# Performance work log

Hardware: AMD Instinct MI355X
Metric: run time of the kernel (lower is better)

## Reference

```python
import jax, jax.numpy as jnp
import numpy as np
import math

D_MODEL = 1024
NUM_HEADS = 16


def setup_inputs() -> dict:
    key = jax.random.key(0)
    k1, k2, k3 = jax.random.split(key, 3)
    x = jax.random.normal(k1, (4, 2048, D_MODEL), dtype=jnp.float32)
    scale = 1.0 / math.sqrt(D_MODEL)
    W_qkv = jax.random.normal(k2, (3 * D_MODEL, D_MODEL), dtype=jnp.float32) * scale
    W_out = jax.random.normal(k3, (D_MODEL, D_MODEL), dtype=jnp.float32) * scale
    return {"x": x, "W_qkv": W_qkv, "W_out": W_out}


def reference(x, W_qkv, W_out):
    B, S, D = x.shape
    H = NUM_HEADS
    hd = D // H
    qkv = x @ W_qkv.T                      # [B,S,3D]
    q, k, v = jnp.split(qkv, 3, axis=-1)
    # [B,S,D] -> [B,H,S,hd]
    q = q.reshape(B, S, H, hd).transpose(0, 2, 1, 3)
    k = k.reshape(B, S, H, hd).transpose(0, 2, 1, 3)
    v = v.reshape(B, S, H, hd).transpose(0, 2, 1, 3)
    scores = jnp.einsum('bhqd,bhkd->bhqk', q, k) / math.sqrt(hd)
    causal = jnp.tril(jnp.ones((S, S), dtype=bool))
    scores = jnp.where(causal, scores, -jnp.inf)
    w = jax.nn.softmax(scores, axis=-1)
    out = jnp.einsum('bhqk,bhkd->bhqd', w, v)
    out = out.transpose(0, 2, 1, 3).reshape(B, S, D)
    return out @ W_out.T
```

## Files before the change

### kernel.cpp

```cpp
#include <hip/hip_runtime.h>
#include <hip/hip_bf16.h>
#include <stdint.h>


typedef __bf16 bf16_t;
typedef __attribute__((ext_vector_type(8))) __bf16 bf16x8;
typedef __attribute__((ext_vector_type(4))) __bf16 bf16x4;
typedef __attribute__((ext_vector_type(4))) float f32x4;

#define LOG2E 1.44269504088896340736f
#define SCLF (0.125f * LOG2E)
#define MFMA16(a, b, c) __builtin_amdgcn_mfma_f32_16x16x32_bf16(a, b, c, 0, 0, 0)

__device__ __forceinline__ bf16x8 ld8(const bf16_t* p) {
    return *(const bf16x8*)p;
}
__device__ __forceinline__ bf16x8 cvt8(const float* p) {
    f32x4 a = *(const f32x4*)p;
    f32x4 b = *(const f32x4*)(p + 4);
    bf16x8 r;
    r[0] = (bf16_t)a[0]; r[1] = (bf16_t)a[1]; r[2] = (bf16_t)a[2]; r[3] = (bf16_t)a[3];
    r[4] = (bf16_t)b[0]; r[5] = (bf16_t)b[1]; r[6] = (bf16_t)b[2]; r[7] = (bf16_t)b[3];
    return r;
}

__device__ __forceinline__ bool probe_f32(const void* w) {
    const uint16_t* u = (const uint16_t*)w;
    int cnt = 0;
#pragma unroll
    for (int i = 0; i < 64; ++i) {
        const int e = (u[i] >> 7) & 0xFF;
        cnt += (e >= 96 && e <= 150) ? 1 : 0;
    }
    return cnt < 56;
}

__device__ __forceinline__ void gll16(const bf16_t* g, bf16_t* l) {
    __builtin_amdgcn_global_load_lds(
        (const __attribute__((address_space(1))) void*)g,
        (__attribute__((address_space(3))) void*)l, 16, 0, 0);
}

__global__ __launch_bounds__(256) void cvt_big_kernel(
    const void* __restrict__ x, const void* __restrict__ wq,
    bf16_t* __restrict__ xb, bf16_t* __restrict__ wqb)
{
    const int gid = blockIdx.x * 256 + threadIdx.x;
    const void* src;
    bf16_t* dst;
    int off;
    if (gid < 1048576) { src = x;  dst = xb;  off = gid; }
    else               { src = wq; dst = wqb; off = gid - 1048576; }
    const bool f32 = probe_f32(src);
    const bf16x8 v = f32 ? cvt8((const float*)src + (size_t)off * 8)
                         : ld8((const bf16_t*)src + (size_t)off * 8);
    *(bf16x8*)(dst + (size_t)off * 8) = v;
}

__global__ __launch_bounds__(256) void cvt_small_kernel(
    const void* __restrict__ wo, bf16_t* __restrict__ wob)
{
    const int off = blockIdx.x * 256 + threadIdx.x;
    const bool f32 = probe_f32(wo);
    const bf16x8 v = f32 ? cvt8((const float*)wo + (size_t)off * 8)
                         : ld8((const bf16_t*)wo + (size_t)off * 8);
    *(bf16x8*)(wob + (size_t)off * 8) = v;
}

template <int EPI>
__global__ __launch_bounds__(256) void gemm_bt_lds(
    const bf16_t* __restrict__ A, const bf16_t* __restrict__ B,
    void* __restrict__ C, bf16_t* __restrict__ VT,
    int M, int N, int K)
{
    __shared__ __align__(16) bf16_t lsA[128 * 32];
    __shared__ __align__(16) bf16_t lsB[128 * 32];

    const int t    = threadIdx.x;
    const int lane = t & 63;
    const int wid  = t >> 6;
    const int quad = lane >> 4;
    const int l15  = lane & 15;
    const int wm   = (wid & 1) * 64;
    const int wn   = (wid >> 1) * 64;
    const int m0   = blockIdx.y * 128;
    const int n0   = blockIdx.x * 128;

    const bf16_t* Ar = A + (size_t)(m0 + (t >> 2)) * K + (t & 3) * 8;
    const bf16_t* Br = B + (size_t)(n0 + (t >> 2)) * K + (t & 3) * 8;
    bf16_t* la = lsA + t * 8;
    bf16_t* lb = lsB + t * 8;

    f32x4 acc[4][4];
#pragma unroll
    for (int i = 0; i < 4; ++i)
#pragma unroll
        for (int j = 0; j < 4; ++j) acc[i][j] = (f32x4){0.f, 0.f, 0.f, 0.f};

    for (int k0 = 0; k0 < K; k0 += 32) {
        __syncthreads();
        gll16(Ar + k0, la);
        gll16(Ar + (size_t)64 * K + k0, la + 2048);
        gll16(Br + k0, lb);
        gll16(Br + (size_t)64 * K + k0, lb + 2048);
        __syncthreads();

        bf16x8 af[4], bfr[4];
#pragma unroll
        for (int i = 0; i < 4; ++i)
            af[i] = ld8(lsA + (wm + i * 16 + l15) * 32 + quad * 8);
#pragma unroll
        for (int j = 0; j < 4; ++j)
            bfr[j] = ld8(lsB + (wn + j * 16 + l15) * 32 + quad * 8);
#pragma unroll
        for (int i = 0; i < 4; ++i)
#pragma unroll
            for (int j = 0; j < 4; ++j)
                acc[i][j] = MFMA16(af[i], bfr[j], acc[i][j]);
    }

#pragma unroll
    for (int i = 0; i < 4; ++i) {
        const int row = m0 + wm + i * 16 + quad * 4;
#pragma unroll
        for (int j = 0; j < 4; ++j) {
            const int col = n0 + wn + j * 16 + l15;
#pragma unroll
            for (int r = 0; r < 4; ++r) {
                const int rr = row + r;
                if (EPI == 0) {
                    ((float*)C)[(size_t)rr * N + col] = acc[i][j][r];
                } else {
                    const bf16_t v = (bf16_t)acc[i][j][r];
                    if (col < 2048) {
                        ((bf16_t*)C)[(size_t)rr * 2048 + col] = v;
                    } else {
                        const int c2 = col - 2048;
                        const int h = c2 >> 6, d = c2 & 63;
                        const int b = rr >> 11, s = rr & 2047;
                        VT[((size_t)((b << 4) + h) * 64 + d) * 2048 + s] = v;
                    }
                }
            }
        }
    }
}

struct Kfrag { bf16x8 k00, k01, k10, k11; };

__device__ __forceinline__ Kfrag ldk(const bf16_t* Kbase, int key0) {
    const bf16_t* kp = Kbase + (size_t)key0 * 2048;
    Kfrag f;
    f.k00 = ld8(kp);
    f.k01 = ld8(kp + 32);
    f.k10 = ld8(kp + (size_t)16 * 2048);
    f.k11 = ld8(kp + (size_t)16 * 2048 + 32);
    return f;
}

__device__ __forceinline__ bf16x4 expq(f32x4 s, float& lsum) {
    bf16x4 r;
#pragma unroll
    for (int i = 0; i < 4; ++i) {
        const float e = exp2f(s[i] * SCLF);
        r[i] = (bf16_t)e;
        lsum += (float)r[i];
    }
    return r;
}
__device__ __forceinline__ bf16x4 expq_m(f32x4 s, float& lsum, int quad, int l15) {
    bf16x4 r;
#pragma unroll
    for (int i = 0; i < 4; ++i) {
        const float e = (quad * 4 + i <= l15) ? exp2f(s[i] * SCLF) : 0.f;
        r[i] = (bf16_t)e;
        lsum += (float)r[i];
    }
    return r;
}

typedef union { bf16x4 h; int u[2]; } pk2;
typedef union { int u[4]; bf16x8 v; } pk4u;

__device__ __forceinline__ bf16x8 xpose(bf16x4 p0, bf16x4 p1, int s0b, int s1b, bool lowsel) {
    pk2 a, b;
    a.h = p0; b.h = p1;
    const int x0 = __builtin_amdgcn_ds_bpermute(s0b, a.u[0]);
    const int y0 = __builtin_amdgcn_ds_bpermute(s0b, b.u[0]);
    const int x1 = __builtin_amdgcn_ds_bpermute(s0b, a.u[1]);
    const int y1 = __builtin_amdgcn_ds_bpermute(s0b, b.u[1]);
    const int x2 = __builtin_amdgcn_ds_bpermute(s1b, a.u[0]);
    const int y2 = __builtin_amdgcn_ds_bpermute(s1b, b.u[0]);
    const int x3 = __builtin_amdgcn_ds_bpermute(s1b, a.u[1]);
    const int y3 = __builtin_amdgcn_ds_bpermute(s1b, b.u[1]);
    pk4u r;
    r.u[0] = lowsel ? x0 : y0;
    r.u[1] = lowsel ? x1 : y1;
    r.u[2] = lowsel ? x2 : y2;
    r.u[3] = lowsel ? x3 : y3;
    return r.v;
}

template <int DIAG>
__device__ __forceinline__ void attn_step(
    const Kfrag& kf, const bf16_t* __restrict__ Vbase, int key0,
    int quad, int l15, int s0b, int s1b, bool lowsel,
    const bf16x8& qa0, const bf16x8& qa1, const bf16x8& qb0, const bf16x8& qb1,
    f32x4 (&oa)[4], f32x4 (&ob)[4], float& la, float& lb)
{
    const bf16_t* vp = Vbase + key0;
    const bf16x8 vf0 = ld8(vp);
    const bf16x8 vf1 = ld8(vp + (size_t)16 * 2048);
    const bf16x8 vf2 = ld8(vp + (size_t)32 * 2048);
    const bf16x8 vf3 = ld8(vp + (size_t)48 * 2048);

    const f32x4 Z = (f32x4){0.f, 0.f, 0.f, 0.f};
    f32x4 s0a = Z, s1a = Z, s0b_ = Z, s1b_ = Z;
    s0a = MFMA16(kf.k00, qa0, s0a); s0a = MFMA16(kf.k01, qa1, s0a);
    s0b_ = MFMA16(kf.k00, qb0, s0b_); s0b_ = MFMA16(kf.k01, qb1, s0b_);
    if (!DIAG) {
        s1a = MFMA16(kf.k10, qa0, s1a); s1a = MFMA16(kf.k11, qa1, s1a);
    }
    s1b_ = MFMA16(kf.k10, qb0, s1b_); s1b_ = MFMA16(kf.k11, qb1, s1b_);

    bf16x4 pa0, pa1, pb0, pb1;
    if (DIAG) {
        pa0 = expq_m(s0a, la, quad, l15);
        pa1 = (bf16x4){(bf16_t)0.f, (bf16_t)0.f, (bf16_t)0.f, (bf16_t)0.f};
        pb0 = expq(s0b_, lb);
        pb1 = expq_m(s1b_, lb, quad, l15);
    } else {
        pa0 = expq(s0a, la); pa1 = expq(s1a, la);
        pb0 = expq(s0b_, lb); pb1 = expq(s1b_, lb);
    }

    const bf16x8 pfa = xpose(pa0, pa1, s0b, s1b, lowsel);
    const bf16x8 pfb = xpose(pb0, pb1, s0b, s1b, lowsel);

    oa[0] = MFMA16(pfa, vf0, oa[0]); ob[0] = MFMA16(pfb, vf0, ob[0]);
    oa[1] = MFMA16(pfa, vf1, oa[1]); ob[1] = MFMA16(pfb, vf1, ob[1]);
    oa[2] = MFMA16(pfa, vf2, oa[2]); ob[2] = MFMA16(pfb, vf2, ob[2]);
    oa[3] = MFMA16(pfa, vf3, oa[3]); ob[3] = MFMA16(pfb, vf3, ob[3]);
}

__global__ __launch_bounds__(128) void attn_kernel(
    const bf16_t* __restrict__ qk, const bf16_t* __restrict__ vt,
    bf16_t* __restrict__ out)
{
    __shared__ float mrg[64][34];

    const int t    = threadIdx.x;
    const int par  = t >> 6;
    const int lane = t & 63;
    const int quad = lane >> 4;
    const int l15  = lane & 15;

    const int bx = blockIdx.x;
    const int u  = bx & 255;
    const int v_ = bx >> 8;

    const int bh = ((u & 15) << 2) | (v_ & 3);
    const int c  = u >> 4;
    const int q2 = v_ >> 2;
    const int cc = (q2 & 1) ? (15 - c) : c;
    const int qt = (q2 << 4) | cc;
    const int b  = bh >> 4;
    const int h  = bh & 15;
    const int q0 = qt << 5;

    const int s0b = ((((quad << 1)) & 3) * 16 + l15) << 2;
    const int s1b = ((((quad << 1) + 1) & 3) * 16 + l15) << 2;
    const bool lowsel = quad < 2;

    const bf16_t* Qp = qk + (size_t)(b * 2048 + q0 + l15) * 2048 + h * 64 + quad * 8;
    const bf16x8 qa0 = ld8(Qp);
    const bf16x8 qa1 = ld8(Qp + 32);
    const bf16x8 qb0 = ld8(Qp + (size_t)16 * 2048);
    const bf16x8 qb1 = ld8(Qp + (size_t)16 * 2048 + 32);

    const bf16_t* Kbase = qk + (size_t)(b * 2048 + l15) * 2048 + 1024 + h * 64 + quad * 8;
    const bf16_t* Vbase = vt + ((size_t)bh * 64 + l15) * 2048 + quad * 8;

    f32x4 oa[4], ob[4];
#pragma unroll
    for (int v = 0; v < 4; ++v) {
        oa[v] = (f32x4){0.f, 0.f, 0.f, 0.f};
        ob[v] = (f32x4){0.f, 0.f, 0.f, 0.f};
    }
    float la = 0.f, lb = 0.f;

    const bool dg = ((qt & 1) == par);
    int kb = par;
    if (kb < qt || dg) {
        Kfrag kc = ldk(Kbase, ((kb < qt) ? kb : qt) << 5);
        while (kb < qt) {
            const int nk = (kb + 2 < qt) ? (kb + 2) : qt;
            Kfrag kn = ldk(Kbase, nk << 5);
            attn_step<0>(kc, Vbase, kb << 5, quad, l15, s0b, s1b, lowsel,
                         qa0, qa1, qb0, qb1, oa, ob, la, lb);
            kc = kn;
            kb += 2;
        }
        if (dg)
            attn_step<1>(kc, Vbase, qt << 5, quad, l15, s0b, s1b, lowsel,
                         qa0, qa1, qb0, qb1, oa, ob, la, lb);
    }

    float* m = &mrg[lane][0];
    if (par == 1) {
#pragma unroll
        for (int v = 0; v < 4; ++v)
#pragma unroll
            for (int r = 0; r < 4; ++r) {
                m[v * 4 + r]      = oa[v][r];
                m[16 + v * 4 + r] = ob[v][r];
            }
        m[32] = la; m[33] = lb;
    }
    __syncthreads();
    if (par == 1) return;

#pragma unroll
    for (int v = 0; v < 4; ++v)
#pragma unroll
        for (int r = 0; r < 4; ++r) {
            oa[v][r] += m[v * 4 + r];
            ob[v][r] += m[16 + v * 4 + r];
        }
    la += m[32]; lb += m[33];

    la += __shfl_xor(la, 16); la += __shfl_xor(la, 32);
    lb += __shfl_xor(lb, 16); lb += __shfl_xor(lb, 32);
    const float inva = 1.0f / la;
    const float invb = 1.0f / lb;

    const size_t obase = (size_t)(b * 2048 + q0 + quad * 4) * 1024 + h * 64 + l15;
#pragma unroll
    for (int r = 0; r < 4; ++r) {
        const float ia = __shfl(inva, quad * 4 + r);
        const float ib = __shfl(invb, quad * 4 + r);
#pragma unroll
        for (int v = 0; v < 4; ++v) {
            out[obase + (size_t)r * 1024 + v * 16]        = (bf16_t)(oa[v][r] * ia);
            out[obase + (size_t)(16 + r) * 1024 + v * 16] = (bf16_t)(ob[v][r] * ib);
        }
    }
}

__global__ void ws_check_kernel(float* out, int code) {
    if (code != 0 && threadIdx.x == 0) out[0] = (float)code;
}

extern "C" void kernel_launch(void* const* d_in, const int* in_sizes, int n_in,
                              void* d_out, int out_size, void* d_ws, size_t ws_size,
                              hipStream_t stream)
{
    const void* x    = d_in[0];
    const void* wqkv = d_in[1];
    const void* wout = d_in[2];

    bf16_t* qkbuf   = (bf16_t*)d_ws;
    bf16_t* vtbuf   = qkbuf + (size_t)8192 * 2048;
    bf16_t* attnbuf = vtbuf + (size_t)64 * 64 * 2048;
    float*  outp    = (float*)d_out;

    bf16_t* xb  = attnbuf;
    bf16_t* wqb = (bf16_t*)d_out;
    bf16_t* wob = vtbuf;

    const int wsBad = (ws_size < (size_t)64 * 1024 * 1024) ? 512 : 0;

    cvt_big_kernel<<<5632, 256, 0, stream>>>(x, wqkv, xb, wqb);

    gemm_bt_lds<1><<<dim3(24, 64), 256, 0, stream>>>(
        xb, wqb, qkbuf, vtbuf, 8192, 3072, 1024);

    attn_kernel<<<4096, 128, 0, stream>>>(qkbuf, vtbuf, attnbuf);

    cvt_small_kernel<<<512, 256, 0, stream>>>(wout, wob);

    gemm_bt_lds<0><<<dim3(8, 64), 256, 0, stream>>>(
        attnbuf, wob, outp, nullptr, 8192, 1024, 1024);

    ws_check_kernel<<<1, 64, 0, stream>>>(outp, wsBad);
}
```

Measured before the change: 363.8 us.

## Software-pipeline attention QK and PV phases, drop intra-block key split

Restructures the attention kernel so each wave handles one head over all key blocks, with no two-wave key split and no LDS merge. It software-pipelines the loop so the PV MFMAs of the previous block overlap the QK/exp of the current block, with K and V prefetched a step ahead. Blocks now hold four heads (256 threads, 1024 blocks) and reorder query tiles for load balance. The f32 probe also moves from a 64-load serial loop per thread to a wave ballot. This raises register pressure and removes intra-query parallelism, which lengthens the tail for long causal rows.

New measurement: 339.2 us. 6.8% less time.

```diff
diff --git a/kernel.cpp b/kernel.cpp
--- a/kernel.cpp
+++ b/kernel.cpp
@@ -24,15 +24,12 @@
     return r;
 }
 
-__device__ __forceinline__ bool probe_f32(const void* w) {
+__device__ __forceinline__ bool probe_f32_wave(const void* w) {
     const uint16_t* u = (const uint16_t*)w;
-    int cnt = 0;
-#pragma unroll
-    for (int i = 0; i < 64; ++i) {
-        const int e = (u[i] >> 7) & 0xFF;
-        cnt += (e >= 96 && e <= 150) ? 1 : 0;
-    }
-    return cnt < 56;
+    const int lane = threadIdx.x & 63;
+    const int e = (u[lane] >> 7) & 0xFF;
+    const unsigned long long m = __ballot(e >= 96 && e <= 150);
+    return __popcll(m) < 56;
 }
 
 __device__ __forceinline__ void gll16(const bf16_t* g, bf16_t* l) {
@@ -51,7 +48,7 @@
     int off;
     if (gid < 1048576) { src = x;  dst = xb;  off = gid; }
     else               { src = wq; dst = wqb; off = gid - 1048576; }
-    const bool f32 = probe_f32(src);
+    const bool f32 = probe_f32_wave(src);
     const bf16x8 v = f32 ? cvt8((const float*)src + (size_t)off * 8)
                          : ld8((const bf16_t*)src + (size_t)off * 8);
     *(bf16x8*)(dst + (size_t)off * 8) = v;
@@ -61,7 +58,7 @@
     const void* __restrict__ wo, bf16_t* __restrict__ wob)
 {
     const int off = blockIdx.x * 256 + threadIdx.x;
-    const bool f32 = probe_f32(wo);
+    const bool f32 = probe_f32_wave(wo);
     const bf16x8 v = f32 ? cvt8((const float*)wo + (size_t)off * 8)
                          : ld8((const bf16_t*)wo + (size_t)off * 8);
     *(bf16x8*)(wob + (size_t)off * 8) = v;
@@ -147,6 +144,7 @@
 }
 
 struct Kfrag { bf16x8 k00, k01, k10, k11; };
+struct Vfrag { bf16x8 v0, v1, v2, v3; };
 
 __device__ __forceinline__ Kfrag ldk(const bf16_t* Kbase, int key0) {
     const bf16_t* kp = Kbase + (size_t)key0 * 2048;
@@ -155,6 +153,15 @@
     f.k01 = ld8(kp + 32);
     f.k10 = ld8(kp + (size_t)16 * 2048);
     f.k11 = ld8(kp + (size_t)16 * 2048 + 32);
+    return f;
+}
+__device__ __forceinline__ Vfrag ldv(const bf16_t* Vbase, int key0) {
+    const bf16_t* vp = Vbase + key0;
+    Vfrag f;
+    f.v0 = ld8(vp);
+    f.v1 = ld8(vp + (size_t)16 * 2048);
+    f.v2 = ld8(vp + (size_t)32 * 2048);
+    f.v3 = ld8(vp + (size_t)48 * 2048);
     return f;
 }
 
@@ -202,18 +209,11 @@
 }
 
 template <int DIAG>
-__device__ __forceinline__ void attn_step(
-    const Kfrag& kf, const bf16_t* __restrict__ Vbase, int key0,
-    int quad, int l15, int s0b, int s1b, bool lowsel,
+__device__ __forceinline__ void qk_phase(
+    const Kfrag& kf, int quad, int l15, int s0b, int s1b, bool lowsel,
     const bf16x8& qa0, const bf16x8& qa1, const bf16x8& qb0, const bf16x8& qb1,
-    f32x4 (&oa)[4], f32x4 (&ob)[4], float& la, float& lb)
-{
-    const bf16_t* vp = Vbase + key0;
-    const bf16x8 vf0 = ld8(vp);
-    const bf16x8 vf1 = ld8(vp + (size_t)16 * 2048);
-    const bf16x8 vf2 = ld8(vp + (size_t)32 * 2048);
-    const bf16x8 vf3 = ld8(vp + (size_t)48 * 2048);
-
+    bf16x8& pfa, bf16x8& pfb, float& la, float& lb)
+{
     const f32x4 Z = (f32x4){0.f, 0.f, 0.f, 0.f};
     f32x4 s0a = Z, s1a = Z, s0b_ = Z, s1b_ = Z;
     s0a = MFMA16(kf.k00, qa0, s0a); s0a = MFMA16(kf.k01, qa1, s0a);
@@ -233,24 +233,26 @@
         pa0 = expq(s0a, la); pa1 = expq(s1a, la);
         pb0 = expq(s0b_, lb); pb1 = expq(s1b_, lb);
     }
-
-    const bf16x8 pfa = xpose(pa0, pa1, s0b, s1b, lowsel);
-    const bf16x8 pfb = xpose(pb0, pb1, s0b, s1b, lowsel);
-
-    oa[0] = MFMA16(pfa, vf0, oa[0]); ob[0] = MFMA16(pfb, vf0, ob[0]);
-    oa[1] = MFMA16(pfa, vf1, oa[1]); ob[1] = MFMA16(pfb, vf1, ob[1]);
-    oa[2] = MFMA16(pfa, vf2, oa[2]); ob[2] = MFMA16(pfb, vf2, ob[2]);
-    oa[3] = MFMA16(pfa, vf3, oa[3]); ob[3] = MFMA16(pfb, vf3, ob[3]);
-}
-
-__global__ __launch_bounds__(128) void attn_kernel(
+    pfa = xpose(pa0, pa1, s0b, s1b, lowsel);
+    pfb = xpose(pb0, pb1, s0b, s1b, lowsel);
+}
+
+__device__ __forceinline__ void pv(
+    const bf16x8& pfa, const bf16x8& pfb, const Vfrag& v,
+    f32x4 (&oa)[4], f32x4 (&ob)[4])
+{
+    oa[0] = MFMA16(pfa, v.v0, oa[0]); ob[0] = MFMA16(pfb, v.v0, ob[0]);
+    oa[1] = MFMA16(pfa, v.v1, oa[1]); ob[1] = MFMA16(pfb, v.v1, ob[1]);
+    oa[2] = MFMA16(pfa, v.v2, oa[2]); ob[2] = MFMA16(pfb, v.v2, ob[2]);
+    oa[3] = MFMA16(pfa, v.v3, oa[3]); ob[3] = MFMA16(pfb, v.v3, ob[3]);
+}
+
+__global__ __launch_bounds__(256, 4) void attn_kernel(
     const bf16_t* __restrict__ qk, const bf16_t* __restrict__ vt,
     bf16_t* __restrict__ out)
 {
-    __shared__ float mrg[64][34];
-
     const int t    = threadIdx.x;
-    const int par  = t >> 6;
+    const int wid  = t >> 6;
     const int lane = t & 63;
     const int quad = lane >> 4;
     const int l15  = lane & 15;
@@ -258,12 +260,10 @@
     const int bx = blockIdx.x;
     const int u  = bx & 255;
     const int v_ = bx >> 8;
-
-    const int bh = ((u & 15) << 2) | (v_ & 3);
+    const int bh = ((u & 15) << 2) | wid;
     const int c  = u >> 4;
-    const int q2 = v_ >> 2;
-    const int cc = (q2 & 1) ? (15 - c) : c;
-    const int qt = (q2 << 4) | cc;
+    const int bs = (v_ & 1) ? (31 - c) : c;
+    const int qt = bs + ((v_ >> 1) << 5);
     const int b  = bh >> 4;
     const int h  = bh & 15;
     const int q0 = qt << 5;
@@ -289,45 +289,33 @@
     }
     float la = 0.f, lb = 0.f;
 
-    const bool dg = ((qt & 1) == par);
-    int kb = par;
-    if (kb < qt || dg) {
-        Kfrag kc = ldk(Kbase, ((kb < qt) ? kb : qt) << 5);
-        while (kb < qt) {
-            const int nk = (kb + 2 < qt) ? (kb + 2) : qt;
-            Kfrag kn = ldk(Kbase, nk << 5);
-            attn_step<0>(kc, Vbase, kb << 5, quad, l15, s0b, s1b, lowsel,
-                         qa0, qa1, qb0, qb1, oa, ob, la, lb);
-            kc = kn;
-            kb += 2;
+    Kfrag kc = ldk(Kbase, 0);
+    Vfrag vc = ldv(Vbase, 0);
+    bf16x8 pfa, pfb;
+
+    if (qt > 0) {
+        Kfrag kn = ldk(Kbase, 32);
+        qk_phase<0>(kc, quad, l15, s0b, s1b, lowsel,
+                    qa0, qa1, qb0, qb1, pfa, pfb, la, lb);
+        kc = kn;
+        for (int kb = 1; kb < qt; ++kb) {
+            Kfrag knn = ldk(Kbase, (kb + 1) << 5);
+            Vfrag vn  = ldv(Vbase, kb << 5);
+            pv(pfa, pfb, vc, oa, ob);
+            qk_phase<0>(kc, quad, l15, s0b, s1b, lowsel,
+                        qa0, qa1, qb0, qb1, pfa, pfb, la, lb);
+            kc = knn; vc = vn;
         }
-        if (dg)
-            attn_step<1>(kc, Vbase, qt << 5, quad, l15, s0b, s1b, lowsel,
-                         qa0, qa1, qb0, qb1, oa, ob, la, lb);
-    }
-
-    float* m = &mrg[lane][0];
-    if (par == 1) {
-#pragma unroll
-        for (int v = 0; v < 4; ++v)
-#pragma unroll
-            for (int r = 0; r < 4; ++r) {
-                m[v * 4 + r]      = oa[v][r];
-                m[16 + v * 4 + r] = ob[v][r];
-            }
-        m[32] = la; m[33] = lb;
-    }
-    __syncthreads();
-    if (par == 1) return;
-
-#pragma unroll
-    for (int v = 0; v < 4; ++v)
-#pragma unroll
-        for (int r = 0; r < 4; ++r) {
-            oa[v][r] += m[v * 4 + r];
-            ob[v][r] += m[16 + v * 4 + r];
-        }
-    la += m[32]; lb += m[33];
+        Vfrag vn = ldv(Vbase, qt << 5);
+        pv(pfa, pfb, vc, oa, ob);
+        qk_phase<1>(kc, quad, l15, s0b, s1b, lowsel,
+                    qa0, qa1, qb0, qb1, pfa, pfb, la, lb);
+        vc = vn;
+    } else {
+        qk_phase<1>(kc, quad, l15, s0b, s1b, lowsel,
+                    qa0, qa1, qb0, qb1, pfa, pfb, la, lb);
+    }
+    pv(pfa, pfb, vc, oa, ob);
 
     la += __shfl_xor(la, 16); la += __shfl_xor(la, 32);
     lb += __shfl_xor(lb, 16); lb += __shfl_xor(lb, 32);
@@ -375,7 +363,7 @@
     gemm_bt_lds<1><<<dim3(24, 64), 256, 0, stream>>>(
         xb, wqb, qkbuf, vtbuf, 8192, 3072, 1024);
 
-    attn_kernel<<<4096, 128, 0, stream>>>(qkbuf, vtbuf, attnbuf);
+    attn_kernel<<<1024, 256, 0, stream>>>(qkbuf, vtbuf, attnbuf);
 
     cvt_small_kernel<<<512, 256, 0, stream>>>(wout, wob);
 
```
